# Kernel optimization log

Measured on AMD Instinct MI355X. Metric: run time of the kernel, lower is better.

## Reference

```python
import jax, jax.numpy as jnp
import numpy as np

HEADS = 8
DIM_HEAD = 64
LN_EPS = 1e-5


def rotate_half(x):
    # pairs (x0,x1) -> (-x1,x0), interleaved layout (einops '(d r)' with r=2)
    x1 = x[..., 0::2]
    x2 = x[..., 1::2]
    return jnp.stack((-x2, x1), axis=-1).reshape(x.shape)


def apply_rope(freqs, x):
    return x * jnp.cos(freqs) + rotate_half(x) * jnp.sin(freqs)


def setup_inputs() -> dict:
    key = jax.random.key(0)
    ks = jax.random.split(key, 4)
    b, n, dim = 2, 4096, 512
    inner = HEADS * DIM_HEAD
    x = jax.random.normal(ks[0], (b, n, dim), dtype=jnp.float32)
    rotary_time_emb = jax.random.uniform(ks[1], (b, n, DIM_HEAD), jnp.float32, 0.0, 6.283185)
    ln_w = jnp.ones((dim,), jnp.float32)
    ln_b = jnp.zeros((dim,), jnp.float32)
    w_qkv = jax.random.normal(ks[2], (inner * 3, dim), jnp.float32) * (dim ** -0.5)
    w_out = jax.random.normal(ks[3], (dim, inner), jnp.float32) * (inner ** -0.5)
    b_out = jnp.zeros((dim,), jnp.float32)
    return dict(x=x, rotary_time_emb=rotary_time_emb, ln_w=ln_w, ln_b=ln_b,
                w_qkv=w_qkv, w_out=w_out, b_out=b_out)


def reference(x, rotary_time_emb, ln_w, ln_b, w_qkv, w_out, b_out):
    b, n, dim = x.shape
    # LayerNorm
    mu = jnp.mean(x, axis=-1, keepdims=True)
    var = jnp.var(x, axis=-1, keepdims=True)
    xn = (x - mu) * jax.lax.rsqrt(var + LN_EPS) * ln_w + ln_b
    # QKV projection (Linear, no bias)
    qkv = xn @ w_qkv.T  # [b, n, 3*inner]
    q, k, v = jnp.split(qkv, 3, axis=-1)

    def to_heads(t):
        return t.reshape(b, n, HEADS, DIM_HEAD).transpose(0, 2, 1, 3)  # b h n d

    q, k, v = to_heads(q), to_heads(k), to_heads(v)
    freqs = rotary_time_emb[:, None, :, :]  # b 1 n d, broadcast over heads
    q = apply_rope(freqs, q)
    k = apply_rope(freqs, k)
    v = apply_rope(freqs, v)  # rotate_value=True
    scale = jnp.asarray(DIM_HEAD ** -0.5, dtype=x.dtype)
    scores = jnp.einsum('bhqd,bhkd->bhqk', q, k) * scale
    attn = jax.nn.softmax(scores, axis=-1)
    out = jnp.einsum('bhqk,bhkd->bhqd', attn, v)
    out = apply_rope(-freqs, out)  # inverse rotation of the output
    out = out.transpose(0, 2, 1, 3).reshape(b, n, HEADS * DIM_HEAD)
    return out @ w_out.T + b_out
```

## Files before the change

### kernel.cpp

```cpp
#include <hip/hip_runtime.h>
#include <cmath>

typedef short bf16x8 __attribute__((ext_vector_type(8)));
typedef float f32x2 __attribute__((ext_vector_type(2)));
typedef float f32x4 __attribute__((ext_vector_type(4)));
typedef float f32x16 __attribute__((ext_vector_type(16)));

#define NSEQ 4096
#define BATCH 2
#define DIM 512
#define HEADS 8
#define NROWS (BATCH * NSEQ)
#define QKVN (3 * DIM)

__device__ __forceinline__ unsigned short f2bf(float f) {
  unsigned int u = __float_as_uint(f);
  u += 0x7fffu + ((u >> 16) & 1u);
  return (unsigned short)(u >> 16);
}
__device__ __forceinline__ float bf2f(unsigned short h) {
  return __uint_as_float(((unsigned int)h) << 16);
}
__device__ __forceinline__ void gload16(const unsigned short* g, unsigned short* l) {
  __builtin_amdgcn_global_load_lds((const __attribute__((address_space(1))) unsigned int*)g,
                                   (__attribute__((address_space(3))) unsigned int*)l, 16, 0, 0);
}

__global__ __launch_bounds__(256) void k_prep(const float* __restrict__ rot,
                                              float* __restrict__ cosT,
                                              float* __restrict__ sinT,
                                              const float* __restrict__ wqkv,
                                              unsigned short* __restrict__ wqkb,
                                              const float* __restrict__ wout,
                                              unsigned short* __restrict__ wob) {
  int bid = blockIdx.x;
  int t = threadIdx.x;
  if (bid < 2048) {
    int i = bid * 256 + t;
    float f = rot[i];
    cosT[i] = cosf(f);
    sinT[i] = sinf(f);
  } else if (bid < 5120) {
    int i = (bid - 2048) * 256 + t;
    wqkb[i] = f2bf(wqkv[i]);
  } else {
    int i = (bid - 5120) * 256 + t;
    wob[i] = f2bf(wout[i]);
  }
}

__global__ __launch_bounds__(256) void k_ln(const float* __restrict__ x,
                                            const float* __restrict__ w,
                                            const float* __restrict__ bb,
                                            unsigned short* __restrict__ xn) {
  int row = blockIdx.x * 4 + (threadIdx.x >> 6);
  int lane = threadIdx.x & 63;
  const float* xr = x + (size_t)row * DIM;
  float v[8];
  float s = 0.f;
#pragma unroll
  for (int j = 0; j < 8; ++j) { v[j] = xr[lane + j * 64]; s += v[j]; }
#pragma unroll
  for (int m = 1; m < 64; m <<= 1) s += __shfl_xor(s, m);
  float mu = s * (1.0f / DIM);
  float q = 0.f;
#pragma unroll
  for (int j = 0; j < 8; ++j) { float d = v[j] - mu; q += d * d; }
#pragma unroll
  for (int m = 1; m < 64; m <<= 1) q += __shfl_xor(q, m);
  float rs = rsqrtf(q * (1.0f / DIM) + 1e-5f);
#pragma unroll
  for (int j = 0; j < 8; ++j) {
    int col = lane + j * 64;
    xn[(size_t)row * DIM + col] = f2bf((v[j] - mu) * rs * w[col] + bb[col]);
  }
}

template <int EPI>
__global__ __launch_bounds__(256) void k_gemm(const unsigned short* __restrict__ A,
                                              const unsigned short* __restrict__ B,
                                              void* __restrict__ C,
                                              const float* __restrict__ bias,
                                              int M, int N, int K) {
  __shared__ __align__(16) unsigned short As[2][128 * 32];
  __shared__ __align__(16) unsigned short Bs[2][128 * 32];
  int bm = blockIdx.x, bn = blockIdx.y;
  int tid = threadIdx.x;
  int lane = tid & 63, w = tid >> 6;
  int wm = (w >> 1) << 6, wn = (w & 1) << 6;
  f32x4 acc[4][4] = {};

#define GSTAGE(KT, BUF) do { \
  _Pragma("unroll") \
  for (int i = 0; i < 2; ++i) { \
    int c = tid + (i << 8); \
    int row = c >> 2, kc = (c & 3) << 3; \
    gload16(A + (size_t)(bm * 128 + row) * K + (KT) + kc, &As[BUF][(w * 64 + i * 256) * 8]); \
    gload16(B + (size_t)(bn * 128 + row) * K + (KT) + kc, &Bs[BUF][(w * 64 + i * 256) * 8]); \
  } } while (0)

  GSTAGE(0, 0);
  __syncthreads();
  int nk = K >> 5;
  for (int t = 0; t < nk; ++t) {
    int cur = t & 1;
    if (t + 1 < nk) GSTAGE((t + 1) << 5, cur ^ 1);
    bf16x8 af[4], bfr[4];
#pragma unroll
    for (int mi = 0; mi < 4; ++mi)
      af[mi] = *(const bf16x8*)&As[cur][(wm + mi * 16 + (lane & 15)) * 32 + ((lane >> 4) << 3)];
#pragma unroll
    for (int ni = 0; ni < 4; ++ni)
      bfr[ni] = *(const bf16x8*)&Bs[cur][(wn + ni * 16 + (lane & 15)) * 32 + ((lane >> 4) << 3)];
#pragma unroll
    for (int mi = 0; mi < 4; ++mi)
#pragma unroll
      for (int ni = 0; ni < 4; ++ni)
        acc[mi][ni] = __builtin_amdgcn_mfma_f32_16x16x32_bf16(af[mi], bfr[ni], acc[mi][ni], 0, 0, 0);
    __syncthreads();
  }
#undef GSTAGE
#pragma unroll
  for (int mi = 0; mi < 4; ++mi) {
#pragma unroll
    for (int ni = 0; ni < 4; ++ni) {
#pragma unroll
      for (int r = 0; r < 4; ++r) {
        int gm = bm * 128 + wm + mi * 16 + ((lane >> 4) << 2) + r;
        int gn = bn * 128 + wn + ni * 16 + (lane & 15);
        if (EPI == 0) {
          ((unsigned short*)C)[(size_t)gm * N + gn] = f2bf(acc[mi][ni][r]);
        } else {
          ((float*)C)[(size_t)gm * N + gn] = acc[mi][ni][r] + bias[gn];
        }
      }
    }
  }
}

__global__ __launch_bounds__(256) void k_rope_split(const unsigned short* __restrict__ qkv,
                                                    const float* __restrict__ cosT,
                                                    const float* __restrict__ sinT,
                                                    unsigned short* __restrict__ qh,
                                                    unsigned short* __restrict__ kh,
                                                    unsigned short* __restrict__ vt) {
  __shared__ unsigned short vs[128][65];
  const float QSC = 0.125f * 1.44269504f;
  int nt = blockIdx.x, bh = blockIdx.y;
  int b = bh >> 3, h = bh & 7;
  int n0 = nt * 128;
  int t = threadIdx.x;
  int sub = t >> 3, cc = t & 7;
#pragma unroll
  for (int rr = 0; rr < 4; ++rr) {
    int row = rr * 32 + sub;
    int n = n0 + row;
    size_t base = ((size_t)(b * NSEQ + n)) * QKVN + h * 64 + cc * 8;
    const float* cb = cosT + ((size_t)(b * NSEQ + n)) * 64 + cc * 8;
    const float* sb = sinT + ((size_t)(b * NSEQ + n)) * 64 + cc * 8;
    float c[8], sn[8];
#pragma unroll
    for (int j = 0; j < 8; ++j) { c[j] = cb[j]; sn[j] = sb[j]; }
    bf16x8 qv = *(const bf16x8*)(qkv + base);
    bf16x8 kv = *(const bf16x8*)(qkv + base + 512);
    bf16x8 vv = *(const bf16x8*)(qkv + base + 1024);
    union { bf16x8 v; unsigned short u[8]; } yq, yk;
#pragma unroll
    for (int j = 0; j < 8; j += 2) {
      {
        float e = bf2f((unsigned short)qv[j]), o = bf2f((unsigned short)qv[j + 1]);
        yq.u[j]     = f2bf((e * c[j] - o * sn[j]) * QSC);
        yq.u[j + 1] = f2bf((o * c[j + 1] + e * sn[j + 1]) * QSC);
      }
      {
        float e = bf2f((unsigned short)kv[j]), o = bf2f((unsigned short)kv[j + 1]);
        yk.u[j]     = f2bf(e * c[j] - o * sn[j]);
        yk.u[j + 1] = f2bf(o * c[j + 1] + e * sn[j + 1]);
      }
      {
        float e = bf2f((unsigned short)vv[j]), o = bf2f((unsigned short)vv[j + 1]);
        vs[row][cc * 8 + j]     = f2bf(e * c[j] - o * sn[j]);
        vs[row][cc * 8 + j + 1] = f2bf(o * c[j + 1] + e * sn[j + 1]);
      }
    }
    *(bf16x8*)(qh + ((size_t)bh * NSEQ + n) * 64 + cc * 8) = yq.v;
    *(bf16x8*)(kh + ((size_t)bh * NSEQ + n) * 64 + cc * 8) = yk.v;
  }
  __syncthreads();
  int d = t >> 2, c4 = t & 3;
#pragma unroll
  for (int g = 0; g < 4; ++g) {
    union { bf16x8 v; unsigned short u[8]; } tv;
#pragma unroll
    for (int j = 0; j < 8; ++j) tv.u[j] = vs[c4 * 32 + g * 8 + j][d];
    *(bf16x8*)(vt + ((size_t)bh * 64 + d) * NSEQ + n0 + c4 * 32 + g * 8) = tv.v;
  }
}

__global__ __launch_bounds__(256, 2) void k_attn(const unsigned short* __restrict__ Qh,
                                                 const unsigned short* __restrict__ Kh,
                                                 const unsigned short* __restrict__ VT,
                                                 unsigned short* __restrict__ opart,
                                                 float* __restrict__ lpart) {
  __shared__ __align__(16) unsigned short Ks[4][64 * 64];
  __shared__ __align__(16) unsigned short Vs[4][64 * 64];
  int bid = blockIdx.x;
  int bh   = (bid & 7) + 8 * ((bid >> 7) & 1);
  int qt   = (bid >> 3) & 15;
  int half = (bid >> 8) & 1;
  int tid = threadIdx.x;
  int w = tid >> 6, lane = tid & 63;
  int lq = lane & 31, hi = lane >> 5;
  int q0 = qt * 256 + w * 64;
  int kv0 = half * 2048;
  int pswap = w >> 1;

  const unsigned short* Kbh = Kh + (size_t)bh * NSEQ * 64;
  const unsigned short* Vbh = VT + (size_t)bh * 64 * NSEQ;

  const unsigned short* QbA = Qh + ((size_t)bh * NSEQ + q0 + lq) * 64 + hi * 8;
  const unsigned short* QbB = QbA + 32 * 64;
  bf16x8 qfA[4], qfB[4];
#pragma unroll
  for (int j = 0; j < 4; ++j) {
    qfA[j] = *(const bf16x8*)(QbA + j * 16);
    qfB[j] = *(const bf16x8*)(QbB + j * 16);
  }

  int c0 = w * 64 + lane;
  int r0 = c0 >> 3, sw0 = ((c0 & 7) ^ (r0 & 7)) << 3;
  int c1 = c0 + 256;
  int r1 = c1 >> 3, sw1 = ((c1 & 7) ^ (r1 & 7)) << 3;
  int ld0 = (w * 64) * 8, ld1 = (256 + w * 64) * 8;

  f32x16 accA0 = (f32x16)0.0f, accA1 = (f32x16)0.0f;
  f32x16 accB0 = (f32x16)0.0f, accB1 = (f32x16)0.0f;
  float lA = 0.f, lB = 0.f;
  int swz = (lq & 7) << 4;

#define STAGE(T, BUF) do { \
  int tg_ = kv0 + (T) * 64; \
  gload16(Kbh + ((size_t)tg_ + r0) * 64 + sw0, &Ks[BUF][ld0]); \
  gload16(Kbh + ((size_t)tg_ + r1) * 64 + sw1, &Ks[BUF][ld1]); \
  gload16(Vbh + (size_t)r0 * NSEQ + tg_ + sw0, &Vs[BUF][ld0]); \
  gload16(Vbh + (size_t)r1 * NSEQ + tg_ + sw1, &Vs[BUF][ld1]); \
} while (0)

  STAGE(0, 0);
  STAGE(1, 1);

  for (int t = 0; t < 32; ++t) {
    int rd = t & 3;
    if (t < 30) {
      STAGE(t + 2, (t + 2) & 3);
      asm volatile("s_waitcnt vmcnt(8)" ::: "memory");
    } else if (t == 30) {
      asm volatile("s_waitcnt vmcnt(4)" ::: "memory");
    } else {
      asm volatile("s_waitcnt vmcnt(0)" ::: "memory");
    }
    __builtin_amdgcn_s_barrier();
    asm volatile("" ::: "memory");
    const char* kb_ = (const char*)&Ks[rd][0];
    const char* vb_ = (const char*)&Vs[rd][0];
#pragma unroll
    for (int pp = 0; pp < 2; ++pp) {
      int ph = pp ^ pswap;
      f32x16 sA = (f32x16)0.0f, sB = (f32x16)0.0f;
      __builtin_amdgcn_s_setprio(1);
#pragma unroll
      for (int j = 0; j < 4; ++j) {
        int cb = j * 32 + hi * 16;
        bf16x8 a = *(const bf16x8*)(kb_ + (ph * 32 + lq) * 128 + (cb ^ swz));
        sA = __builtin_amdgcn_mfma_f32_32x32x16_bf16(a, qfA[j], sA, 0, 0, 0);
        sB = __builtin_amdgcn_mfma_f32_32x32x16_bf16(a, qfB[j], sB, 0, 0, 0);
      }
      __builtin_amdgcn_s_setprio(0);
#pragma unroll
      for (int r = 0; r < 16; ++r) sA[r] = __builtin_amdgcn_exp2f(sA[r]);
#pragma unroll
      for (int r = 0; r < 16; ++r) sB[r] = __builtin_amdgcn_exp2f(sB[r]);
      {
        union { f32x16 v; f32x2 p[8]; } ua, ub; ua.v = sA; ub.v = sB;
        f32x2 a01 = ua.p[0] + ua.p[1], a23 = ua.p[2] + ua.p[3];
        f32x2 a45 = ua.p[4] + ua.p[5], a67 = ua.p[6] + ua.p[7];
        f32x2 ta = (a01 + a23) + (a45 + a67);
        lA += ta.x + ta.y;
        f32x2 b01 = ub.p[0] + ub.p[1], b23 = ub.p[2] + ub.p[3];
        f32x2 b45 = ub.p[4] + ub.p[5], b67 = ub.p[6] + ub.p[7];
        f32x2 tb = (b01 + b23) + (b45 + b67);
        lB += tb.x + tb.y;
      }
      unsigned int dwA[8], dwB[8];
#pragma unroll
      for (int m = 0; m < 8; ++m) {
        asm("v_cvt_pk_bf16_f32 %0, %1, %2" : "=v"(dwA[m]) : "v"(sA[2 * m]), "v"(sA[2 * m + 1]));
        asm("v_cvt_pk_bf16_f32 %0, %1, %2" : "=v"(dwB[m]) : "v"(sB[2 * m]), "v"(sB[2 * m + 1]));
      }
      __builtin_amdgcn_s_setprio(1);
#pragma unroll
      for (int kk = 0; kk < 2; ++kk) {
        const int B = 4 * kk;
        unsigned int svA0 = hi ? dwA[B + 0] : dwA[B + 2];
        unsigned int svA1 = hi ? dwA[B + 1] : dwA[B + 3];
        unsigned int svB0 = hi ? dwB[B + 0] : dwB[B + 2];
        unsigned int svB1 = hi ? dwB[B + 1] : dwB[B + 3];
        unsigned int rvA0 = (unsigned int)__shfl_xor((int)svA0, 32);
        unsigned int rvA1 = (unsigned int)__shfl_xor((int)svA1, 32);
        unsigned int rvB0 = (unsigned int)__shfl_xor((int)svB0, 32);
        unsigned int rvB1 = (unsigned int)__shfl_xor((int)svB1, 32);
        union { unsigned int d[4]; bf16x8 v; } puA, puB;
        puA.d[0] = hi ? rvA0 : dwA[B + 0];
        puA.d[1] = hi ? rvA1 : dwA[B + 1];
        puA.d[2] = hi ? dwA[B + 2] : rvA0;
        puA.d[3] = hi ? dwA[B + 3] : rvA1;
        puB.d[0] = hi ? rvB0 : dwB[B + 0];
        puB.d[1] = hi ? rvB1 : dwB[B + 1];
        puB.d[2] = hi ? dwB[B + 2] : rvB0;
        puB.d[3] = hi ? dwB[B + 3] : rvB1;
        int cb = (ph * 2 + kk) * 32 + hi * 16;
        bf16x8 v0 = *(const bf16x8*)(vb_ + lq * 128 + (cb ^ swz));
        bf16x8 v1 = *(const bf16x8*)(vb_ + (32 + lq) * 128 + (cb ^ swz));
        accA0 = __builtin_amdgcn_mfma_f32_32x32x16_bf16(v0, puA.v, accA0, 0, 0, 0);
        accA1 = __builtin_amdgcn_mfma_f32_32x32x16_bf16(v1, puA.v, accA1, 0, 0, 0);
        accB0 = __builtin_amdgcn_mfma_f32_32x32x16_bf16(v0, puB.v, accB0, 0, 0, 0);
        accB1 = __builtin_amdgcn_mfma_f32_32x32x16_bf16(v1, puB.v, accB1, 0, 0, 0);
      }
      __builtin_amdgcn_s_setprio(0);
    }
  }
#undef STAGE

  float lsumA = lA + __shfl_xor(lA, 32);
  float lsumB = lB + __shfl_xor(lB, 32);
  size_t qrowA = (size_t)(half * 16 + bh) * NSEQ + q0 + lq;
  size_t qrowB = qrowA + 32;
  if (hi == 0) {
    lpart[qrowA] = lsumA;
    lpart[qrowB] = lsumB;
  }
  unsigned short* obA = opart + qrowA * 64;
  unsigned short* obB = opart + qrowB * 64;
#pragma unroll
  for (int rg = 0; rg < 4; ++rg) {
    unsigned int pa0[2], pa1[2], pb0[2], pb1[2];
    asm("v_cvt_pk_bf16_f32 %0, %1, %2" : "=v"(pa0[0]) : "v"(accA0[4 * rg + 0]), "v"(accA0[4 * rg + 1]));
    asm("v_cvt_pk_bf16_f32 %0, %1, %2" : "=v"(pa0[1]) : "v"(accA0[4 * rg + 2]), "v"(accA0[4 * rg + 3]));
    asm("v_cvt_pk_bf16_f32 %0, %1, %2" : "=v"(pa1[0]) : "v"(accA1[4 * rg + 0]), "v"(accA1[4 * rg + 1]));
    asm("v_cvt_pk_bf16_f32 %0, %1, %2" : "=v"(pa1[1]) : "v"(accA1[4 * rg + 2]), "v"(accA1[4 * rg + 3]));
    asm("v_cvt_pk_bf16_f32 %0, %1, %2" : "=v"(pb0[0]) : "v"(accB0[4 * rg + 0]), "v"(accB0[4 * rg + 1]));
    asm("v_cvt_pk_bf16_f32 %0, %1, %2" : "=v"(pb0[1]) : "v"(accB0[4 * rg + 2]), "v"(accB0[4 * rg + 3]));
    asm("v_cvt_pk_bf16_f32 %0, %1, %2" : "=v"(pb1[0]) : "v"(accB1[4 * rg + 0]), "v"(accB1[4 * rg + 1]));
    asm("v_cvt_pk_bf16_f32 %0, %1, %2" : "=v"(pb1[1]) : "v"(accB1[4 * rg + 2]), "v"(accB1[4 * rg + 3]));
    *(uint2*)(obA + 8 * rg + 4 * hi) = *(uint2*)pa0;
    *(uint2*)(obA + 32 + 8 * rg + 4 * hi) = *(uint2*)pa1;
    *(uint2*)(obB + 8 * rg + 4 * hi) = *(uint2*)pb0;
    *(uint2*)(obB + 32 + 8 * rg + 4 * hi) = *(uint2*)pb1;
  }
}

__global__ __launch_bounds__(256) void k_combine(const unsigned short* __restrict__ opart,
                                                 const float* __restrict__ lpart,
                                                 const float* __restrict__ cosT,
                                                 const float* __restrict__ sinT,
                                                 unsigned short* __restrict__ ao) {
  int bh = blockIdx.y;
  int b = bh >> 3, h = bh & 7;
  int t = threadIdx.x;
  int q = blockIdx.x * 16 + (t >> 4);
  int d = (t & 15) * 4;
  size_t i0 = (size_t)bh * NSEQ + q;
  const size_t HOFF = (size_t)16 * NSEQ;
  float l = lpart[i0] + lpart[i0 + HOFF];
  float o[4] = {0.f, 0.f, 0.f, 0.f};
#pragma unroll
  for (int p = 0; p < 2; ++p) {
    uint2 u = *(const uint2*)(opart + (i0 + p * HOFF) * 64 + d);
    o[0] += bf2f((unsigned short)(u.x & 0xffff));
    o[1] += bf2f((unsigned short)(u.x >> 16));
    o[2] += bf2f((unsigned short)(u.y & 0xffff));
    o[3] += bf2f((unsigned short)(u.y >> 16));
  }
  float inv = 1.0f / l;
  float4 c4 = *(const float4*)(cosT + ((size_t)b * NSEQ + q) * 64 + d);
  float4 s4 = *(const float4*)(sinT + ((size_t)b * NSEQ + q) * 64 + d);
  float yx = o[0] * inv;
  float yy = o[1] * inv;
  float yz = o[2] * inv;
  float yw = o[3] * inv;
  float r0 = yx * c4.x + yy * s4.x;
  float r1 = yy * c4.y - yx * s4.y;
  float r2 = yz * c4.z + yw * s4.z;
  float r3 = yw * c4.w - yz * s4.w;
  unsigned int w0, w1;
  asm("v_cvt_pk_bf16_f32 %0, %1, %2" : "=v"(w0) : "v"(r0), "v"(r1));
  asm("v_cvt_pk_bf16_f32 %0, %1, %2" : "=v"(w1) : "v"(r2), "v"(r3));
  unsigned int uu[2] = {w0, w1};
  *(uint2*)(ao + ((size_t)b * NSEQ + q) * DIM + h * 64 + d) = *(uint2*)uu;
}

extern "C" void kernel_launch(void* const* d_in, const int* in_sizes, int n_in,
                              void* d_out, int out_size, void* d_ws, size_t ws_size,
                              hipStream_t stream) {
  const float* x    = (const float*)d_in[0];
  const float* rot  = (const float*)d_in[1];
  const float* lnw  = (const float*)d_in[2];
  const float* lnb  = (const float*)d_in[3];
  const float* wqkv = (const float*)d_in[4];
  const float* wout = (const float*)d_in[5];
  const float* bout = (const float*)d_in[6];
  float* out = (float*)d_out;

  char* ws = (char*)d_ws;
  const size_t MB = (size_t)1 << 20;
  float* cosT          = (float*)(ws + 0 * MB);
  float* sinT          = (float*)(ws + 2 * MB);
  unsigned short* wqkb = (unsigned short*)(ws + 4 * MB);
  float* lpart         = (float*)(ws + 5 * MB + 512 * 1024);
  unsigned short* wob  = (unsigned short*)(ws + 6 * MB);
  unsigned short* xn   = (unsigned short*)(ws + 8 * MB);
  unsigned short* opart = (unsigned short*)(ws + 8 * MB);
  unsigned short* qkv  = (unsigned short*)(ws + 16 * MB);
  unsigned short* qh   = (unsigned short*)(ws + 40 * MB);
  unsigned short* ao   = (unsigned short*)(ws + 40 * MB);
  unsigned short* kh   = (unsigned short*)(ws + 48 * MB);
  unsigned short* vt   = (unsigned short*)(ws + 56 * MB);

  k_prep<<<6144, 256, 0, stream>>>(rot, cosT, sinT, wqkv, wqkb, wout, wob);
  k_ln<<<NROWS / 4, 256, 0, stream>>>(x, lnw, lnb, xn);
  k_gemm<0><<<dim3(NROWS / 128, QKVN / 128), 256, 0, stream>>>(xn, wqkb, qkv, nullptr,
                                                               NROWS, QKVN, DIM);
  k_rope_split<<<dim3(NSEQ / 128, 16), 256, 0, stream>>>(qkv, cosT, sinT, qh, kh, vt);
  k_attn<<<512, 256, 0, stream>>>(qh, kh, vt, opart, lpart);
  k_combine<<<dim3(NSEQ / 16, 16), 256, 0, stream>>>(opart, lpart, cosT, sinT, ao);
  k_gemm<1><<<dim3(NROWS / 128, DIM / 128), 256, 0, stream>>>(ao, wob, out, bout,
                                                              NROWS, DIM, DIM);
}
```

Baseline: 141.0 us.

## Fuse layernorm into prep kernel, use hardware sincos, shrink out-proj GEMM tile

Moves the LayerNorm into the prep kernel as extra blocks, which removes one kernel launch. Cos and sin are now computed with the hardware sin/cos builtins on the angle prescaled by 1/2pi, in place of the libm cosf and sinf, at some cost in accuracy. The output projection GEMM uses a 64-row M tile so it launches twice as many blocks and fills the CUs better. The attention kernel also drops the per-wave phase swap of the K sub-tile order.

```diff
diff --git a/kernel.cpp b/kernel.cpp
--- a/kernel.cpp
+++ b/kernel.cpp
@@ -32,70 +32,81 @@
                                               const float* __restrict__ wqkv,
                                               unsigned short* __restrict__ wqkb,
                                               const float* __restrict__ wout,
-                                              unsigned short* __restrict__ wob) {
+                                              unsigned short* __restrict__ wob,
+                                              const float* __restrict__ x,
+                                              const float* __restrict__ lnw,
+                                              const float* __restrict__ lnb,
+                                              unsigned short* __restrict__ xn) {
+  const float INV2PI = 0.15915494309f;
   int bid = blockIdx.x;
   int t = threadIdx.x;
   if (bid < 2048) {
     int i = bid * 256 + t;
-    float f = rot[i];
-    cosT[i] = cosf(f);
-    sinT[i] = sinf(f);
+    float rv = rot[i] * INV2PI;
+    cosT[i] = __builtin_amdgcn_cosf(rv);
+    sinT[i] = __builtin_amdgcn_sinf(rv);
   } else if (bid < 5120) {
     int i = (bid - 2048) * 256 + t;
     wqkb[i] = f2bf(wqkv[i]);
-  } else {
+  } else if (bid < 6144) {
     int i = (bid - 5120) * 256 + t;
     wob[i] = f2bf(wout[i]);
-  }
-}
-
-__global__ __launch_bounds__(256) void k_ln(const float* __restrict__ x,
-                                            const float* __restrict__ w,
-                                            const float* __restrict__ bb,
-                                            unsigned short* __restrict__ xn) {
-  int row = blockIdx.x * 4 + (threadIdx.x >> 6);
-  int lane = threadIdx.x & 63;
-  const float* xr = x + (size_t)row * DIM;
-  float v[8];
-  float s = 0.f;
-#pragma unroll
-  for (int j = 0; j < 8; ++j) { v[j] = xr[lane + j * 64]; s += v[j]; }
-#pragma unroll
-  for (int m = 1; m < 64; m <<= 1) s += __shfl_xor(s, m);
-  float mu = s * (1.0f / DIM);
-  float q = 0.f;
-#pragma unroll
-  for (int j = 0; j < 8; ++j) { float d = v[j] - mu; q += d * d; }
-#pragma unroll
-  for (int m = 1; m < 64; m <<= 1) q += __shfl_xor(q, m);
-  float rs = rsqrtf(q * (1.0f / DIM) + 1e-5f);
-#pragma unroll
-  for (int j = 0; j < 8; ++j) {
-    int col = lane + j * 64;
-    xn[(size_t)row * DIM + col] = f2bf((v[j] - mu) * rs * w[col] + bb[col]);
-  }
-}
-
-template <int EPI>
+  } else {
+    int row = (bid - 6144) * 4 + (t >> 6);
+    int lane = t & 63;
+    const float* xr = x + (size_t)row * DIM;
+    float v[8];
+    float s = 0.f;
+#pragma unroll
+    for (int j = 0; j < 8; ++j) { v[j] = xr[lane + j * 64]; s += v[j]; }
+#pragma unroll
+    for (int m = 1; m < 64; m <<= 1) s += __shfl_xor(s, m);
+    float mu = s * (1.0f / DIM);
+    float q = 0.f;
+#pragma unroll
+    for (int j = 0; j < 8; ++j) { float d = v[j] - mu; q += d * d; }
+#pragma unroll
+    for (int m = 1; m < 64; m <<= 1) q += __shfl_xor(q, m);
+    float rs = rsqrtf(q * (1.0f / DIM) + 1e-5f);
+#pragma unroll
+    for (int j = 0; j < 8; ++j) {
+      int col = lane + j * 64;
+      xn[(size_t)row * DIM + col] = f2bf((v[j] - mu) * rs * lnw[col] + lnb[col]);
+    }
+  }
+}
+
+template <int EPI, int TM>
 __global__ __launch_bounds__(256) void k_gemm(const unsigned short* __restrict__ A,
                                               const unsigned short* __restrict__ B,
                                               void* __restrict__ C,
                                               const float* __restrict__ bias,
                                               int M, int N, int K) {
-  __shared__ __align__(16) unsigned short As[2][128 * 32];
+  constexpr int MI = TM / 32;
+  __shared__ __align__(16) unsigned short As[2][TM * 32];
   __shared__ __align__(16) unsigned short Bs[2][128 * 32];
   int bm = blockIdx.x, bn = blockIdx.y;
   int tid = threadIdx.x;
   int lane = tid & 63, w = tid >> 6;
-  int wm = (w >> 1) << 6, wn = (w & 1) << 6;
-  f32x4 acc[4][4] = {};
+  int wm = (w >> 1) * (TM / 2), wn = (w & 1) << 6;
+  f32x4 acc[MI][4] = {};
 
 #define GSTAGE(KT, BUF) do { \
+  if constexpr (TM == 128) { \
+    _Pragma("unroll") \
+    for (int i = 0; i < 2; ++i) { \
+      int c = tid + (i << 8); \
+      int row = c >> 2, kc = (c & 3) << 3; \
+      gload16(A + (size_t)(bm * 128 + row) * K + (KT) + kc, &As[BUF][(w * 64 + i * 256) * 8]); \
+    } \
+  } else { \
+    int row = tid >> 2, kc = (tid & 3) << 3; \
+    gload16(A + (size_t)(bm * 64 + row) * K + (KT) + kc, &As[BUF][(w * 64) * 8]); \
+  } \
   _Pragma("unroll") \
   for (int i = 0; i < 2; ++i) { \
     int c = tid + (i << 8); \
     int row = c >> 2, kc = (c & 3) << 3; \
-    gload16(A + (size_t)(bm * 128 + row) * K + (KT) + kc, &As[BUF][(w * 64 + i * 256) * 8]); \
     gload16(B + (size_t)(bn * 128 + row) * K + (KT) + kc, &Bs[BUF][(w * 64 + i * 256) * 8]); \
   } } while (0)
 
@@ -105,15 +116,15 @@
   for (int t = 0; t < nk; ++t) {
     int cur = t & 1;
     if (t + 1 < nk) GSTAGE((t + 1) << 5, cur ^ 1);
-    bf16x8 af[4], bfr[4];
-#pragma unroll
-    for (int mi = 0; mi < 4; ++mi)
+    bf16x8 af[MI], bfr[4];
+#pragma unroll
+    for (int mi = 0; mi < MI; ++mi)
       af[mi] = *(const bf16x8*)&As[cur][(wm + mi * 16 + (lane & 15)) * 32 + ((lane >> 4) << 3)];
 #pragma unroll
     for (int ni = 0; ni < 4; ++ni)
       bfr[ni] = *(const bf16x8*)&Bs[cur][(wn + ni * 16 + (lane & 15)) * 32 + ((lane >> 4) << 3)];
 #pragma unroll
-    for (int mi = 0; mi < 4; ++mi)
+    for (int mi = 0; mi < MI; ++mi)
 #pragma unroll
       for (int ni = 0; ni < 4; ++ni)
         acc[mi][ni] = __builtin_amdgcn_mfma_f32_16x16x32_bf16(af[mi], bfr[ni], acc[mi][ni], 0, 0, 0);
@@ -121,12 +132,12 @@
   }
 #undef GSTAGE
 #pragma unroll
-  for (int mi = 0; mi < 4; ++mi) {
+  for (int mi = 0; mi < MI; ++mi) {
 #pragma unroll
     for (int ni = 0; ni < 4; ++ni) {
 #pragma unroll
       for (int r = 0; r < 4; ++r) {
-        int gm = bm * 128 + wm + mi * 16 + ((lane >> 4) << 2) + r;
+        int gm = bm * TM + wm + mi * 16 + ((lane >> 4) << 2) + r;
         int gn = bn * 128 + wn + ni * 16 + (lane & 15);
         if (EPI == 0) {
           ((unsigned short*)C)[(size_t)gm * N + gn] = f2bf(acc[mi][ni][r]);
@@ -213,7 +224,6 @@
   int lq = lane & 31, hi = lane >> 5;
   int q0 = qt * 256 + w * 64;
   int kv0 = half * 2048;
-  int pswap = w >> 1;
 
   const unsigned short* Kbh = Kh + (size_t)bh * NSEQ * 64;
   const unsigned short* Vbh = VT + (size_t)bh * 64 * NSEQ;
@@ -264,8 +274,7 @@
     const char* kb_ = (const char*)&Ks[rd][0];
     const char* vb_ = (const char*)&Vs[rd][0];
 #pragma unroll
-    for (int pp = 0; pp < 2; ++pp) {
-      int ph = pp ^ pswap;
+    for (int ph = 0; ph < 2; ++ph) {
       f32x16 sA = (f32x16)0.0f, sB = (f32x16)0.0f;
       __builtin_amdgcn_s_setprio(1);
 #pragma unroll
@@ -426,13 +435,13 @@
   unsigned short* kh   = (unsigned short*)(ws + 48 * MB);
   unsigned short* vt   = (unsigned short*)(ws + 56 * MB);
 
-  k_prep<<<6144, 256, 0, stream>>>(rot, cosT, sinT, wqkv, wqkb, wout, wob);
-  k_ln<<<NROWS / 4, 256, 0, stream>>>(x, lnw, lnb, xn);
-  k_gemm<0><<<dim3(NROWS / 128, QKVN / 128), 256, 0, stream>>>(xn, wqkb, qkv, nullptr,
-                                                               NROWS, QKVN, DIM);
+  k_prep<<<8192, 256, 0, stream>>>(rot, cosT, sinT, wqkv, wqkb, wout, wob,
+                                   x, lnw, lnb, xn);
+  k_gemm<0, 128><<<dim3(NROWS / 128, QKVN / 128), 256, 0, stream>>>(xn, wqkb, qkv, nullptr,
+                                                                    NROWS, QKVN, DIM);
   k_rope_split<<<dim3(NSEQ / 128, 16), 256, 0, stream>>>(qkv, cosT, sinT, qh, kh, vt);
   k_attn<<<512, 256, 0, stream>>>(qh, kh, vt, opart, lpart);
   k_combine<<<dim3(NSEQ / 16, 16), 256, 0, stream>>>(opart, lpart, cosT, sinT, ao);
-  k_gemm<1><<<dim3(NROWS / 128, DIM / 128), 256, 0, stream>>>(ao, wob, out, bout,
-                                                              NROWS, DIM, DIM);
-}
+  k_gemm<1, 64><<<dim3(NROWS / 64, DIM / 128), 256, 0, stream>>>(ao, wob, out, bout,
+                                                                 NROWS, DIM, DIM);
+}
```

Result: faster. 136.0 us (-3.5%).
